# Kernel tuning notes

Measured on AMD Instinct MI355X. Metric: run time of the kernel, lower is better.

## Reference

```python
import jax, jax.numpy as jnp
import numpy as np

IN_C, OUT_C, K, STRIDE, PAD, N_EXPERTS = 64, 128, 3, 1, 1, 4
B, H, W = 32, 64, 64


def setup_inputs() -> dict:
    key = jax.random.key(0)
    k1, k2, k3, k4 = jax.random.split(key, 4)
    x = jax.random.normal(k1, (B, IN_C, H, W), dtype=jnp.float32)
    idx = jax.random.randint(k2, (B,), 0, N_EXPERTS, dtype=jnp.int64)
    # Expert conv weights/biases (PyTorch Conv2d layout: [out_c, in_c, kh, kw])
    fan_in = IN_C * K * K
    bound = 1.0 / np.sqrt(fan_in)
    Wc = jax.random.uniform(k3, (N_EXPERTS, OUT_C, IN_C, K, K), dtype=jnp.float32,
                            minval=-bound, maxval=bound)
    bc = jax.random.uniform(k4, (N_EXPERTS, OUT_C), dtype=jnp.float32,
                            minval=-bound, maxval=bound)
    return {"x": x, "idx": idx, "Wc": Wc, "bc": bc}


def _conv2d(x, w, b):
    # x: [B, C_in, H, W], w: [C_out, C_in, K, K], b: [C_out]
    y = jax.lax.conv_general_dilated(
        x, w,
        window_strides=(STRIDE, STRIDE),
        padding=[(PAD, PAD), (PAD, PAD)],
        dimension_numbers=("NCHW", "OIHW", "NCHW"),
    )
    return y + b[None, :, None, None]


def reference(x, idx, Wc, bc):
    # Compute every expert's conv for every sample (faithful to the torch code),
    # then gather each sample's selected expert output.
    results = jax.vmap(lambda w, b: _conv2d(x, w, b))(Wc, bc)  # [E, B, C_out, H, W]
    results = jnp.moveaxis(results, 0, 1)                      # [B, E, C_out, H, W]
    out = jnp.take_along_axis(
        results, idx[:, None, None, None, None].astype(jnp.int32), axis=1
    )  # [B, 1, C_out, H, W]
    return jnp.squeeze(out, axis=1)
```

## Files before the change

kernel.cpp:

```cpp
#include <hip/hip_runtime.h>
#include <hip/hip_bf16.h>


#define IC 64
#define OC 128
#define HH 64
#define WW 64

typedef short short8 __attribute__((ext_vector_type(8)));
typedef ushort ushort8 __attribute__((ext_vector_type(8)));
typedef float float16 __attribute__((ext_vector_type(16)));

typedef const __attribute__((address_space(1))) void gas_t;
typedef __attribute__((address_space(3))) void las_t;

static __device__ __forceinline__ ushort f2bf(float v) {
    __hip_bfloat16 h = __float2bfloat16(v);
    return *(ushort*)&h;
}

__global__ __launch_bounds__(256)
void reorder_w(const float* __restrict__ Wc, ushort* __restrict__ wout) {
    __shared__ ushort lw[4 * 584];
    const int t   = threadIdx.x;
    const int e   = blockIdx.x >> 5;
    const int oc0 = (blockIdx.x & 31) * 4;
    const float* src = Wc + (size_t)(e * 128 + oc0) * 576;
#pragma unroll
    for (int k = 0; k < 9; ++k) {
        const int f   = k * 256 + t;
        const int ocl = f / 576;
        const int rem = f - ocl * 576;
        lw[ocl * 584 + rem] = f2bf(src[f]);
    }
    __syncthreads();
#pragma unroll
    for (int k = 0; k < 2; ++k) {
        const int n = k * 256 + t;
        if (n < 288) {
            const int ocl = n & 3, ich = (n >> 2) & 7, tap = n >> 5;
            ushort8 v;
#pragma unroll
            for (int icl = 0; icl < 8; ++icl)
                v[icl] = lw[ocl * 584 + (ich * 8 + icl) * 9 + tap];
            *(ushort8*)(wout +
                ((((size_t)(e * 9 + tap) * 8 + ich) * 128 + oc0 + ocl) * 8)) = v;
        }
    }
}

__global__ __launch_bounds__(512, 2)
void moe_conv_mfma(const float* __restrict__ x, const int* __restrict__ idx,
                   const ushort* __restrict__ wre, const float* __restrict__ bc,
                   float* __restrict__ out) {
    __shared__ __align__(16) ushort xs[10 * 8 * 66 * 8];
    __shared__ __align__(16) ushort wbuf[2][8192];
    __shared__ float bias[128];

    const int t = threadIdx.x;

    const int lin = blockIdx.x;
    const int nw  = (lin & 7) * 32 + (lin >> 3);
    const int b   = nw >> 3;
    const int rq  = nw & 7;
    const int row0 = rq * 8;
    const int e    = ((unsigned)idx[b]) & 3;

    const int lane31 = t & 31;
    const int lhi    = (t >> 5) & 1;
    const int wv     = t >> 6;

    const ushort* we = wre + (size_t)e * 9 * 8192;

#pragma unroll
    for (int i = 0; i < 2; ++i) {
        __builtin_amdgcn_global_load_lds(
            (gas_t*)(we + i * 4096 + t * 8),
            (las_t*)&wbuf[0][i * 4096 + t * 8], 16, 0, 0);
    }

    if (t < 320) {
        const int r = t >> 5, rem = t & 31;
        const int ich = rem >> 2, side = (rem >> 1) & 1, q = rem & 1;
        const int hc = side ? 65 : 0;
        ushort4 z = {0, 0, 0, 0};
        *(ushort4*)&xs[(((r * 8 + ich) * 66 + hc) * 8 + q * 4)] = z;
    } else if (t < 448) {
        bias[t - 320] = bc[e * OC + (t - 320)];
    }

    const float* xb = x + (size_t)b * IC * HH * WW;
    {
        const int gc   = t & 63;
        const int csel = t >> 6;
#pragma unroll
        for (int it = 0; it < 20; ++it) {
            const int combo = it * 8 + csel;
            const int r = combo >> 4, rem = combo & 15;
            const int ich = rem >> 1, q = rem & 1;
            const int gr = row0 - 1 + r;
            ushort4 u = {0, 0, 0, 0};
            if ((unsigned)gr < (unsigned)HH) {
                const int ic0 = ich * 8 + q * 4;
                u.x = f2bf(xb[((ic0 + 0) * HH + gr) * WW + gc]);
                u.y = f2bf(xb[((ic0 + 1) * HH + gr) * WW + gc]);
                u.z = f2bf(xb[((ic0 + 2) * HH + gr) * WW + gc]);
                u.w = f2bf(xb[((ic0 + 3) * HH + gr) * WW + gc]);
            }
            *(ushort4*)&xs[(((r * 8 + ich) * 66 + (gc + 1)) * 8 + q * 4)] = u;
        }
    }

    float16 acc[4][2];
#pragma unroll
    for (int g = 0; g < 4; ++g)
#pragma unroll
        for (int cg = 0; cg < 2; ++cg)
#pragma unroll
            for (int r = 0; r < 16; ++r) acc[g][cg][r] = 0.0f;

    const int xrow  = wv * 4224 + lane31 * 8;
    const int abase = lane31 * 8;

#pragma unroll
    for (int tap = 0; tap < 9; ++tap) {
        const int cur = tap & 1;
        if (tap < 8) {
            const ushort* wt = we + (tap + 1) * 8192;
#pragma unroll
            for (int i = 0; i < 2; ++i) {
                __builtin_amdgcn_global_load_lds(
                    (gas_t*)(wt + i * 4096 + t * 8),
                    (las_t*)&wbuf[cur ^ 1][i * 4096 + t * 8], 16, 0, 0);
            }
            asm volatile("s_waitcnt vmcnt(2) lgkmcnt(0)" ::: "memory");
        } else {
            asm volatile("s_waitcnt vmcnt(0) lgkmcnt(0)" ::: "memory");
        }
        __builtin_amdgcn_s_barrier();

        const int kh = tap / 3;
        const int kw = tap - kh * 3;
        const int xtap = xrow + kh * 4224 + kw * 8;

        __builtin_amdgcn_s_setprio(1);
#pragma unroll
        for (int ks = 0; ks < 4; ++ks) {
            const int ich = ks * 2 + lhi;
            const int xo = xtap + ich * 528;
            const short8 b0 = *(const short8*)&xs[xo];
            const short8 b1 = *(const short8*)&xs[xo + 256];
            const int ao = abase + ich * 1024;
            const short8 a0 = *(const short8*)&wbuf[cur][ao];
            const short8 a1 = *(const short8*)&wbuf[cur][ao + 256];
            const short8 a2 = *(const short8*)&wbuf[cur][ao + 512];
            const short8 a3 = *(const short8*)&wbuf[cur][ao + 768];
            acc[0][0] = __builtin_amdgcn_mfma_f32_32x32x16_bf16(a0, b0, acc[0][0], 0, 0, 0);
            acc[0][1] = __builtin_amdgcn_mfma_f32_32x32x16_bf16(a0, b1, acc[0][1], 0, 0, 0);
            acc[1][0] = __builtin_amdgcn_mfma_f32_32x32x16_bf16(a1, b0, acc[1][0], 0, 0, 0);
            acc[1][1] = __builtin_amdgcn_mfma_f32_32x32x16_bf16(a1, b1, acc[1][1], 0, 0, 0);
            acc[2][0] = __builtin_amdgcn_mfma_f32_32x32x16_bf16(a2, b0, acc[2][0], 0, 0, 0);
            acc[2][1] = __builtin_amdgcn_mfma_f32_32x32x16_bf16(a2, b1, acc[2][1], 0, 0, 0);
            acc[3][0] = __builtin_amdgcn_mfma_f32_32x32x16_bf16(a3, b0, acc[3][0], 0, 0, 0);
            acc[3][1] = __builtin_amdgcn_mfma_f32_32x32x16_bf16(a3, b1, acc[3][1], 0, 0, 0);
        }
        __builtin_amdgcn_s_setprio(0);

        if (tap < 8)
            __builtin_amdgcn_s_barrier();
    }

#pragma unroll
    for (int g = 0; g < 4; ++g) {
        const int ocb = g * 32 + 4 * lhi;
#pragma unroll
        for (int reg = 0; reg < 16; ++reg) {
            const int oc = ocb + (reg & 3) + 8 * (reg >> 2);
            const float bv = bias[oc];
            const size_t base = (((size_t)b * OC + oc) * HH + (row0 + wv)) * WW;
            out[base + lane31]      = acc[g][0][reg] + bv;
            out[base + 32 + lane31] = acc[g][1][reg] + bv;
        }
    }
}

extern "C" void kernel_launch(void* const* d_in, const int* in_sizes, int n_in,
                              void* d_out, int out_size, void* d_ws, size_t ws_size,
                              hipStream_t stream) {
    const float* x   = (const float*)d_in[0];
    const int*   idx = (const int*)d_in[1];
    const float* Wc  = (const float*)d_in[2];
    const float* bc  = (const float*)d_in[3];
    float* out  = (float*)d_out;
    ushort* wre = (ushort*)d_ws;

    reorder_w<<<128, 256, 0, stream>>>(Wc, wre);
    moe_conv_mfma<<<256, 512, 0, stream>>>(x, idx, wre, bc, out);
}
```

Measured before the change: 112.2 us.

## Precompute bf16 channel-interleaved x in prep kernel and async-load into LDS

The prep kernel now also converts x to bf16 in a [b][row][ich][w][8] layout in the workspace. The conv kernel then fills its LDS input tile with 16-byte global_load_lds transfers instead of strided fp32 loads followed by in-register conversion. The goal is to cut the scattered load and convert cost in the main kernel and to overlap the input fill with the weight prefetch. In exchange, x is read once and written once as bf16 in an extra pass, and halo rows are re-read by neighbouring blocks.

Result: slower. 116.3 us (+3.7%).

```diff
diff --git a/kernel.cpp b/kernel.cpp
--- a/kernel.cpp
+++ b/kernel.cpp
@@ -7,6 +7,8 @@
 #define HH 64
 #define WW 64
 
+#define XPRE 524288
+
 typedef short short8 __attribute__((ext_vector_type(8)));
 typedef ushort ushort8 __attribute__((ext_vector_type(8)));
 typedef float float16 __attribute__((ext_vector_type(16)));
@@ -20,39 +22,60 @@
 }
 
 __global__ __launch_bounds__(256)
-void reorder_w(const float* __restrict__ Wc, ushort* __restrict__ wout) {
-    __shared__ ushort lw[4 * 584];
+void prep(const float* __restrict__ x, const float* __restrict__ Wc,
+          ushort* __restrict__ ws) {
+    const int bid = blockIdx.x;
     const int t   = threadIdx.x;
-    const int e   = blockIdx.x >> 5;
-    const int oc0 = (blockIdx.x & 31) * 4;
-    const float* src = Wc + (size_t)(e * 128 + oc0) * 576;
-#pragma unroll
-    for (int k = 0; k < 9; ++k) {
-        const int f   = k * 256 + t;
-        const int ocl = f / 576;
-        const int rem = f - ocl * 576;
-        lw[ocl * 584 + rem] = f2bf(src[f]);
-    }
-    __syncthreads();
-#pragma unroll
-    for (int k = 0; k < 2; ++k) {
-        const int n = k * 256 + t;
-        if (n < 288) {
-            const int ocl = n & 3, ich = (n >> 2) & 7, tap = n >> 5;
-            ushort8 v;
-#pragma unroll
-            for (int icl = 0; icl < 8; ++icl)
-                v[icl] = lw[ocl * 584 + (ich * 8 + icl) * 9 + tap];
-            *(ushort8*)(wout +
-                ((((size_t)(e * 9 + tap) * 8 + ich) * 128 + oc0 + ocl) * 8)) = v;
+    if (bid < 2048) {
+        __shared__ ushort lx[4096];
+        const int b = bid >> 6, h = bid & 63;
+        const int w = t & 63;
+        const float* xb = x + (size_t)b * 262144 + (size_t)h * 64 + w;
+#pragma unroll
+        for (int j = 0; j < 16; ++j) {
+            const int ic = (t >> 6) * 16 + j;
+            lx[((ic >> 3) * 64 + w) * 8 + (ic & 7)] = f2bf(xb[(size_t)ic * 4096]);
+        }
+        __syncthreads();
+        ushort* ox = ws + XPRE + (size_t)bid * 4096;
+#pragma unroll
+        for (int k = 0; k < 2; ++k) {
+            const int c = k * 256 + t;
+            *(ushort8*)(ox + c * 8) = *(ushort8*)(lx + c * 8);
+        }
+    } else {
+        __shared__ ushort lw[4 * 584];
+        const int bid2 = bid - 2048;
+        const int e   = bid2 >> 5;
+        const int oc0 = (bid2 & 31) * 4;
+        const float* src = Wc + (size_t)(e * 128 + oc0) * 576;
+#pragma unroll
+        for (int k = 0; k < 9; ++k) {
+            const int f   = k * 256 + t;
+            const int ocl = f / 576;
+            const int rem = f - ocl * 576;
+            lw[ocl * 584 + rem] = f2bf(src[f]);
+        }
+        __syncthreads();
+#pragma unroll
+        for (int k = 0; k < 2; ++k) {
+            const int n = k * 256 + t;
+            if (n < 288) {
+                const int ocl = n & 3, ich = (n >> 2) & 7, tap = n >> 5;
+                ushort8 v;
+#pragma unroll
+                for (int icl = 0; icl < 8; ++icl)
+                    v[icl] = lw[ocl * 584 + (ich * 8 + icl) * 9 + tap];
+                *(ushort8*)(ws +
+                    ((((size_t)(e * 9 + tap) * 8 + ich) * 128 + oc0 + ocl) * 8)) = v;
+            }
         }
     }
 }
 
 __global__ __launch_bounds__(512, 2)
-void moe_conv_mfma(const float* __restrict__ x, const int* __restrict__ idx,
-                   const ushort* __restrict__ wre, const float* __restrict__ bc,
-                   float* __restrict__ out) {
+void moe_conv_mfma(const ushort* __restrict__ ws, const int* __restrict__ idx,
+                   const float* __restrict__ bc, float* __restrict__ out) {
     __shared__ __align__(16) ushort xs[10 * 8 * 66 * 8];
     __shared__ __align__(16) ushort wbuf[2][8192];
     __shared__ float bias[128];
@@ -67,16 +90,47 @@
     const int e    = ((unsigned)idx[b]) & 3;
 
     const int lane31 = t & 31;
+    const int lane64 = t & 63;
     const int lhi    = (t >> 5) & 1;
     const int wv     = t >> 6;
 
-    const ushort* we = wre + (size_t)e * 9 * 8192;
+    const ushort* we = ws + (size_t)e * 9 * 8192;
 
 #pragma unroll
     for (int i = 0; i < 2; ++i) {
         __builtin_amdgcn_global_load_lds(
             (gas_t*)(we + i * 4096 + t * 8),
             (las_t*)&wbuf[0][i * 4096 + t * 8], 16, 0, 0);
+    }
+
+    const ushort* xpre_b = ws + XPRE + (size_t)b * 262144;
+#pragma unroll
+    for (int ich = 0; ich < 8; ++ich) {
+        const int gr = row0 - 1 + wv;
+        ushort* dst = &xs[((wv * 8 + ich) * 66 + 1) * 8];
+        if ((unsigned)gr < 64u) {
+            __builtin_amdgcn_global_load_lds(
+                (gas_t*)(xpre_b + ((size_t)gr * 8 + ich) * 512 + lane64 * 8),
+                (las_t*)dst, 16, 0, 0);
+        } else {
+            ushort8 z = {0, 0, 0, 0, 0, 0, 0, 0};
+            *(ushort8*)(dst + lane64 * 8) = z;
+        }
+    }
+#pragma unroll
+    for (int k = 0; k < 2; ++k) {
+        const int ei = wv * 2 + k;
+        const int r  = 8 + (ei >> 3), ich = ei & 7;
+        const int gr = row0 - 1 + r;
+        ushort* dst = &xs[((r * 8 + ich) * 66 + 1) * 8];
+        if ((unsigned)gr < 64u) {
+            __builtin_amdgcn_global_load_lds(
+                (gas_t*)(xpre_b + ((size_t)gr * 8 + ich) * 512 + lane64 * 8),
+                (las_t*)dst, 16, 0, 0);
+        } else {
+            ushort8 z = {0, 0, 0, 0, 0, 0, 0, 0};
+            *(ushort8*)(dst + lane64 * 8) = z;
+        }
     }
 
     if (t < 320) {
@@ -87,28 +141,6 @@
         *(ushort4*)&xs[(((r * 8 + ich) * 66 + hc) * 8 + q * 4)] = z;
     } else if (t < 448) {
         bias[t - 320] = bc[e * OC + (t - 320)];
-    }
-
-    const float* xb = x + (size_t)b * IC * HH * WW;
-    {
-        const int gc   = t & 63;
-        const int csel = t >> 6;
-#pragma unroll
-        for (int it = 0; it < 20; ++it) {
-            const int combo = it * 8 + csel;
-            const int r = combo >> 4, rem = combo & 15;
-            const int ich = rem >> 1, q = rem & 1;
-            const int gr = row0 - 1 + r;
-            ushort4 u = {0, 0, 0, 0};
-            if ((unsigned)gr < (unsigned)HH) {
-                const int ic0 = ich * 8 + q * 4;
-                u.x = f2bf(xb[((ic0 + 0) * HH + gr) * WW + gc]);
-                u.y = f2bf(xb[((ic0 + 1) * HH + gr) * WW + gc]);
-                u.z = f2bf(xb[((ic0 + 2) * HH + gr) * WW + gc]);
-                u.w = f2bf(xb[((ic0 + 3) * HH + gr) * WW + gc]);
-            }
-            *(ushort4*)&xs[(((r * 8 + ich) * 66 + (gc + 1)) * 8 + q * 4)] = u;
-        }
     }
 
     float16 acc[4][2];
@@ -192,8 +224,8 @@
     const float* Wc  = (const float*)d_in[2];
     const float* bc  = (const float*)d_in[3];
     float* out  = (float*)d_out;
-    ushort* wre = (ushort*)d_ws;
-
-    reorder_w<<<128, 256, 0, stream>>>(Wc, wre);
-    moe_conv_mfma<<<256, 512, 0, stream>>>(x, idx, wre, bc, out);
-}
+    ushort* ws  = (ushort*)d_ws;
+
+    prep<<<2176, 256, 0, stream>>>(x, Wc, ws);
+    moe_conv_mfma<<<256, 512, 0, stream>>>(ws, idx, bc, out);
+}
```
